# Performance work log

Hardware: AMD Instinct MI355X
Metric: run time of the kernel (lower is better)

Reference implementation:

```python
import jax, jax.numpy as jnp
import numpy as np

N, E, F_IN, H, C, G, NCLS, L = 50000, 600000, 128, 4, 64, 64, 3, 3
HC = H * C  # 256


def gatv2_layer(x, src, dst, Wl, bl, Wr, br, att, bias):
    # PyG GATv2Conv (concat=True, negative_slope=0.2, share_weights=False),
    # eval mode so attention dropout is identity.
    n = x.shape[0]
    xl = (x @ Wl + bl).reshape(n, H, C)  # source transform
    xr = (x @ Wr + br).reshape(n, H, C)  # target transform
    e = jax.nn.leaky_relu(xl[src] + xr[dst], negative_slope=0.2)  # [E',H,C]
    score = jnp.einsum('ehc,hc->eh', e, att)                      # [E',H]
    # softmax over incoming edges of each destination node
    mx = jax.ops.segment_max(score, dst, num_segments=n)
    ex = jnp.exp(score - mx[dst])
    denom = jax.ops.segment_sum(ex, dst, num_segments=n)
    alpha = ex / denom[dst]                                       # [E',H]
    out = jax.ops.segment_sum(alpha[..., None] * xl[src], dst, num_segments=n)
    return out.reshape(n, HC) + bias


def setup_inputs() -> dict:
    key = jax.random.key(0)
    ks = jax.random.split(key, 32)
    d = {}
    d['x'] = jax.random.normal(ks[0], (N, F_IN), dtype=jnp.float32)
    d['edge_index'] = jax.random.randint(ks[1], (2, E), 0, N, dtype=jnp.int64)
    d['batch'] = jnp.sort(jax.random.randint(ks[2], (N,), 0, G, dtype=jnp.int64))
    k = 3
    for li in range(L):
        fin = F_IN if li == 0 else HC
        s = 1.0 / np.sqrt(fin)
        d[f'Wl{li}'] = jax.random.normal(ks[k], (fin, HC), dtype=jnp.float32) * s; k += 1
        d[f'bl{li}'] = jnp.zeros((HC,), dtype=jnp.float32)
        d[f'Wr{li}'] = jax.random.normal(ks[k], (fin, HC), dtype=jnp.float32) * s; k += 1
        d[f'br{li}'] = jnp.zeros((HC,), dtype=jnp.float32)
        d[f'att{li}'] = jax.random.normal(ks[k], (H, C), dtype=jnp.float32) * (1.0 / np.sqrt(C)); k += 1
        d[f'bias{li}'] = jnp.zeros((HC,), dtype=jnp.float32)
    d['Wout'] = jax.random.normal(ks[k], (HC, NCLS), dtype=jnp.float32) * (1.0 / np.sqrt(HC))
    d['bout'] = jnp.zeros((NCLS,), dtype=jnp.float32)
    return d


def reference(x, edge_index, batch,
              Wl0, bl0, Wr0, br0, att0, bias0,
              Wl1, bl1, Wr1, br1, att1, bias1,
              Wl2, bl2, Wr2, br2, att2, bias2,
              Wout, bout):
    # add self loops (add_self_loops=True)
    loops = jnp.arange(N, dtype=edge_index.dtype)
    src = jnp.concatenate([edge_index[0], loops])
    dst = jnp.concatenate([edge_index[1], loops])

    h = gatv2_layer(x, src, dst, Wl0, bl0, Wr0, br0, att0, bias0)
    for (Wl, bl, Wr, br, att, bias) in [(Wl1, bl1, Wr1, br1, att1, bias1),
                                        (Wl2, bl2, Wr2, br2, att2, bias2)]:
        h = jax.nn.relu(h)
        h = gatv2_layer(h, src, dst, Wl, bl, Wr, br, att, bias)

    # pooling=0: mean + max over graphs
    counts = jax.ops.segment_sum(jnp.ones((N,), dtype=h.dtype), batch, num_segments=G)
    mean_p = jax.ops.segment_sum(h, batch, num_segments=G) / jnp.maximum(counts, 1.0)[:, None]
    max_p = jax.ops.segment_max(h, batch, num_segments=G)
    p = mean_p + max_p
    # dropout is identity in eval mode
    logits = p @ Wout + bout
    return jax.nn.softmax(logits, axis=1)
```

## Files before the change

kernel.cpp:

```cpp
#include <hip/hip_runtime.h>
#include <math.h>

#define N_NODES 50000
#define N_EDGES 600000
#define F_INPUT 128
#define HCDIM 256
#define NGRAPH 64
#define NCLS 3
#define MPAD 50048
#define SCAN_NB ((N_NODES + 255) / 256)
#define LOG2E 1.4426950408889634f
#define NPART 32
#define COLX_PAD 16
#define TOTAL_E (N_EDGES + N_NODES)
#define PLANE64 ((size_t)N_NODES * 64)
#define EDGE_CHUNKS ((N_NODES + 63) / 64)
#define DBINS 64
#define BSEG (SCAN_NB / 4)
#define GEMM_NB ((MPAD / 64) * 4)
#define GEMM_QPX (GEMM_NB / 8)

#define FILL_NB   ((TOTAL_E + COLX_PAD + 255) / 256)
#define SPLITX_NB (MPAD * F_INPUT / 4 / 256)
#define ZERO_NB   (((MPAD - N_NODES) * HCDIM / 4 + 255) / 256)
#define WPREP_NB  (512 * (F_INPUT + HCDIM + HCDIM) / 256)
#define PREP_NB   (SPLITX_NB + ZERO_NB + WPREP_NB)
#define HIST_NB   ((N_EDGES + N_NODES + 255) / 256)
#define BND_NB    ((N_NODES + 255) / 256)

typedef float f32x4 __attribute__((ext_vector_type(4)));
typedef float f32x2 __attribute__((ext_vector_type(2)));
typedef _Float16 f16x8 __attribute__((ext_vector_type(8)));
typedef _Float16 f16x4 __attribute__((ext_vector_type(4)));
typedef _Float16 h2 __attribute__((ext_vector_type(2)));

__device__ __forceinline__ void gl_lds16(const void* g, void* l) {
    __builtin_amdgcn_global_load_lds(
        (const __attribute__((address_space(1))) unsigned int*)g,
        (__attribute__((address_space(3))) unsigned int*)l, 16, 0, 0);
}

__device__ __forceinline__ h2 bch2(unsigned int u) { return __builtin_bit_cast(h2, u); }
__device__ __forceinline__ h2 pk16(float a, float b) {
    return __builtin_bit_cast(h2, __builtin_amdgcn_cvt_pkrtz(a, b));
}

__device__ __forceinline__ float quad_reduce_add(float p) {
    int s1 = __builtin_amdgcn_update_dpp(0, __builtin_bit_cast(int, p), 0xB1, 0xF, 0xF, true);
    p += __builtin_bit_cast(float, s1);
    int s2 = __builtin_amdgcn_update_dpp(0, __builtin_bit_cast(int, p), 0x4E, 0xF, 0xF, true);
    p += __builtin_bit_cast(float, s2);
    return p;
}

__global__ void hist_boundary_kernel(const int* __restrict__ ei, int* __restrict__ deg,
                                     const int* __restrict__ batch,
                                     int* __restrict__ startg, int* __restrict__ endg) {
    int b = blockIdx.x;
    if (b < HIST_NB) {
        int i = b * 256 + threadIdx.x;
        int total = N_EDGES + N_NODES;
        if (i >= total) return;
        int d = (i < N_EDGES) ? ei[N_EDGES + i] : (i - N_EDGES);
        atomicAdd(&deg[d], 1);
    } else {
        int i = (b - HIST_NB) * 256 + threadIdx.x;
        if (i >= N_NODES) return;
        int g = batch[i];
        if (i == 0 || batch[i - 1] != g) startg[g] = i;
        if (i == N_NODES - 1 || batch[i + 1] != g) endg[g] = i + 1;
    }
}

__global__ void block_scan_kernel(const int* __restrict__ deg, int* __restrict__ rowptr,
                                  int* __restrict__ bsums) {
    __shared__ int wt[4];
    int b = blockIdx.x, t = threadIdx.x, lane = t & 63, wid = t >> 6;
    int i = b * 256 + t;
    int v = (i < N_NODES) ? deg[i] : 0;
    int x = v;
    #pragma unroll
    for (int off = 1; off < 64; off <<= 1) {
        int y = __shfl_up(x, off, 64);
        if (lane >= off) x += y;
    }
    if (lane == 63) wt[wid] = x;
    __syncthreads();
    if (t == 0) {
        int s = 0;
        #pragma unroll
        for (int j = 0; j < 4; ++j) { int tv = wt[j]; wt[j] = s; s += tv; }
        bsums[b] = s;
    }
    __syncthreads();
    if (i < N_NODES) rowptr[i] = wt[wid] + x - v;
}

__global__ void add_off_kernel(int* __restrict__ rowptr, int* __restrict__ cursor,
                               const int* __restrict__ bsums,
                               const int* __restrict__ deg, int* __restrict__ dhist,
                               int* __restrict__ bcnt) {
    __shared__ int red[256];
    __shared__ int lh[DBINS];
    int b = blockIdx.x, t = threadIdx.x;
    if (t < DBINS) lh[t] = 0;
    red[t] = (t < b) ? bsums[t] : 0;
    __syncthreads();
    for (int off = 128; off > 0; off >>= 1) {
        if (t < off) red[t] += red[t + off];
        __syncthreads();
    }
    int offv = red[0];
    int i = b * 256 + t;
    if (i < N_NODES) {
        int r = rowptr[i] + offv;
        rowptr[i] = r;
        cursor[i] = r;
        int dg = deg[i];
        atomicAdd(&lh[dg < (DBINS - 1) ? dg : (DBINS - 1)], 1);
    }
    if (i == 0) rowptr[N_NODES] = N_EDGES + N_NODES;
    __syncthreads();
    if (t < DBINS) {
        bcnt[b * DBINS + t] = lh[t];
        if (lh[t] != 0) atomicAdd(&dhist[t], lh[t]);
    }
}

__global__ __launch_bounds__(256) void binscan_kernel(const int* __restrict__ dhist,
                                                      int* __restrict__ bcnt) {
    __shared__ int sb[SCAN_NB * DBINS];
    __shared__ int part[4][DBINS];
    __shared__ int binstart[DBINS];
    int t = threadIdx.x;
    for (int i = t; i < SCAN_NB * DBINS; i += 256) sb[i] = bcnt[i];
    if (t < 64) {
        int x = dhist[t];
        #pragma unroll
        for (int off = 1; off < 64; off <<= 1) {
            int y = __shfl_up(x, off, 64);
            if (t >= off) x += y;
        }
        int total = __shfl(x, 63, 64);
        binstart[t] = total - x;
    }
    __syncthreads();
    int l = t & 63, seg = t >> 6;
    int ps = 0;
    for (int b = seg * BSEG; b < (seg + 1) * BSEG; ++b) ps += sb[b * DBINS + l];
    part[seg][l] = ps;
    __syncthreads();
    int off = binstart[l];
    for (int s = 0; s < seg; ++s) off += part[s][l];
    for (int b = seg * BSEG; b < (seg + 1) * BSEG; ++b) {
        int tv = sb[b * DBINS + l];
        sb[b * DBINS + l] = off;
        off += tv;
    }
    __syncthreads();
    for (int i = t; i < SCAN_NB * DBINS; i += 256) bcnt[i] = sb[i];
}

__global__ void prep_fill_kernel(
    const int* __restrict__ ei, int* __restrict__ cursor, int* __restrict__ colx,
    const int* __restrict__ deg, const int* __restrict__ rowptr,
    const int* __restrict__ bcnt, int2* __restrict__ meta,
    const float* __restrict__ x, _Float16* __restrict__ A,
    _Float16* __restrict__ Bt0, _Float16* __restrict__ Bt1, _Float16* __restrict__ Bt2,
    const float* __restrict__ Wl0, const float* __restrict__ Wr0,
    const float* __restrict__ Wl1, const float* __restrict__ Wr1,
    const float* __restrict__ Wl2, const float* __restrict__ Wr2)
{
    int b = blockIdx.x;
    if (b < FILL_NB) {
        __shared__ int lcnt[DBINS];
        int t = threadIdx.x;
        int i = b * 256 + t;
        if (b < SCAN_NB) {
            if (t < DBINS) lcnt[t] = 0;
            __syncthreads();
            if (i < N_NODES) {
                int dg = deg[i];
                int bin = dg < (DBINS - 1) ? dg : (DBINS - 1);
                int myr = atomicAdd(&lcnt[bin], 1);
                int pos = bcnt[b * DBINS + bin] + myr;
                meta[pos] = make_int2(i, rowptr[i] | (dg << 20));
            }
        }
        if (i < TOTAL_E) {
            int s, d;
            if (i < N_EDGES) { s = ei[i]; d = ei[N_EDGES + i]; }
            else             { s = i - N_EDGES; d = s; }
            int pos = atomicAdd(&cursor[d], 1);
            colx[pos] = s * 64;
        } else if (i < TOTAL_E + COLX_PAD) {
            colx[i] = 0;
        }
        return;
    }
    b -= FILL_NB;
    if (b < SPLITX_NB) {
        int base = (b * 256 + threadIdx.x) * 4;
        int row = base >> 7;
        float4 v = make_float4(0.f, 0.f, 0.f, 0.f);
        if (row < N_NODES) v = *(const float4*)&x[base];
        f16x4 o;
        o.x = (_Float16)v.x; o.y = (_Float16)v.y; o.z = (_Float16)v.z; o.w = (_Float16)v.w;
        *(f16x4*)&A[base] = o;
    } else if (b < SPLITX_NB + ZERO_NB) {
        int i = ((b - SPLITX_NB) * 256 + threadIdx.x) * 4;
        if (i < (MPAD - N_NODES) * HCDIM) {
            f16x4 z = {(_Float16)0.f, (_Float16)0.f, (_Float16)0.f, (_Float16)0.f};
            *(f16x4*)&A[(size_t)N_NODES * HCDIM + i] = z;
        }
    } else {
        int t = (b - SPLITX_NB - ZERO_NB) * 256 + threadIdx.x;
        const float* Wl; const float* Wr; _Float16* Bt; int K;
        if (t < 512 * F_INPUT)            { Wl = Wl0; Wr = Wr0; Bt = Bt0; K = F_INPUT; }
        else if (t < 512 * (F_INPUT + HCDIM)) { t -= 512 * F_INPUT; Wl = Wl1; Wr = Wr1; Bt = Bt1; K = HCDIM; }
        else                              { t -= 512 * (F_INPUT + HCDIM); Wl = Wl2; Wr = Wr2; Bt = Bt2; K = HCDIM; }
        int n = t & 511, k = t >> 9;
        float w = (n < 256) ? Wl[k * 256 + n] : Wr[k * 256 + (n - 256)];
        Bt[n * K + k] = (_Float16)w;
    }
}

__global__ __launch_bounds__(256) void gemm_mfma(
    const _Float16* __restrict__ A, const _Float16* __restrict__ B,
    int K,
    const float* __restrict__ bl, const float* __restrict__ br,
    unsigned char* __restrict__ xl8, _Float16* __restrict__ xrh)
{
    __shared__ _Float16 sA[64 * 64], sB[128 * 64];
    int tid = threadIdx.x;
    int lane = tid & 63, wave = tid >> 6;
    int wm = wave >> 1, wn = wave & 1;
    int bid = blockIdx.x;
    int lin = (bid & 7) * GEMM_QPX + (bid >> 3);
    int bx = lin >> 2, by = lin & 3;
    int row0 = bx * 64;
    int n0 = by * 128;
    int quad = lane >> 4, l16 = lane & 15;

    f32x4 acc[2][4];
    #pragma unroll
    for (int i = 0; i < 2; ++i)
        #pragma unroll
        for (int j = 0; j < 4; ++j)
            acc[i][j] = (f32x4){0.f, 0.f, 0.f, 0.f};

    for (int k0 = 0; k0 < K; k0 += 64) {
        __syncthreads();
        #pragma unroll
        for (int pass = 0; pass < 2; ++pass) {
            int c = tid + pass * 256;
            int r = c >> 3;
            int pl = c & 7;
            int pg = pl ^ (r & 7);
            size_t ga = (size_t)(row0 + r) * K + k0 + pg * 8;
            gl_lds16(A + ga, sA + c * 8);
        }
        #pragma unroll
        for (int pass = 0; pass < 4; ++pass) {
            int c = tid + pass * 256;
            int r = c >> 3;
            int pl = c & 7;
            int pg = pl ^ (r & 7);
            size_t gb = (size_t)(n0 + r) * K + k0 + pg * 8;
            gl_lds16(B + gb, sB + c * 8);
        }
        __syncthreads();

        #pragma unroll
        for (int kk = 0; kk < 2; ++kk) {
            f16x8 fa[2], fb[4];
            #pragma unroll
            for (int i = 0; i < 2; ++i) {
                int rr = wm * 32 + i * 16 + l16;
                int ca = (kk * 4 + quad) ^ (rr & 7);
                fa[i] = *(const f16x8*)&sA[rr * 64 + ca * 8];
            }
            #pragma unroll
            for (int j = 0; j < 4; ++j) {
                int nn = wn * 64 + j * 16 + l16;
                int cb = (kk * 4 + quad) ^ (nn & 7);
                fb[j] = *(const f16x8*)&sB[nn * 64 + cb * 8];
            }
            #pragma unroll
            for (int i = 0; i < 2; ++i)
                #pragma unroll
                for (int j = 0; j < 4; ++j)
                    acc[i][j] = __builtin_amdgcn_mfma_f32_16x16x32_f16(fa[i], fb[j], acc[i][j], 0, 0, 0);
        }
    }

    if (by < 2) {
        int cb0 = by * 128;
        #pragma unroll
        for (int j = 0; j < 4; ++j) {
            int col = cb0 + wn * 64 + j * 16 + l16;
            float bj = bl[col];
            int hh = col >> 6, c64 = col & 63;
            unsigned char* xlp = xl8 + (size_t)hh * PLANE64;
            #pragma unroll
            for (int i = 0; i < 2; ++i) {
                int rbase = row0 + wm * 32 + i * 16 + quad * 4;
                #pragma unroll
                for (int r = 0; r < 4; ++r) {
                    int row = rbase + r;
                    if (row < N_NODES) {
                        float v = acc[i][j][r] + bj;
                        int pk = __builtin_amdgcn_cvt_pk_fp8_f32(v, v, 0, false);
                        xlp[(size_t)row * 64 + c64] = (unsigned char)pk;
                    }
                }
            }
        }
    } else {
        int cb0 = (by - 2) * 128;
        #pragma unroll
        for (int j = 0; j < 4; ++j) {
            int col = cb0 + wn * 64 + j * 16 + l16;
            float bj = br[col];
            int hh = col >> 6, c64 = col & 63;
            _Float16* xrp = xrh + (size_t)hh * PLANE64;
            #pragma unroll
            for (int i = 0; i < 2; ++i) {
                int rbase = row0 + wm * 32 + i * 16 + quad * 4;
                #pragma unroll
                for (int r = 0; r < 4; ++r) {
                    int row = rbase + r;
                    if (row < N_NODES)
                        xrp[(size_t)row * 64 + c64] = (_Float16)(acc[i][j][r] + bj);
                }
            }
        }
    }
}

__global__ __launch_bounds__(256) void gat_edge(
    const unsigned char* __restrict__ xl8, const _Float16* __restrict__ xrh,
    const float* __restrict__ att, const float* __restrict__ bias,
    const int2* __restrict__ meta, const int* __restrict__ colx,
    _Float16* __restrict__ outh, _Float16* __restrict__ onext, int mode)
{
    int head = blockIdx.x & 3;
    int chunk = blockIdx.x >> 2;
    int wave = threadIdx.x >> 6;
    int lane = threadIdx.x & 63;
    int g  = lane >> 2;
    int ll = lane & 3;
    int slot = chunk * 64 + wave * 16 + g;
    bool valid = slot < N_NODES;
    int saddr = valid ? slot : 0;
    int2 m = meta[saddr];
    int node = m.x;
    int e0 = m.y & 0xFFFFF;
    int cnt = valid ? (int)((unsigned)m.y >> 20) : 0;
    int ch0 = head * 64 + ll * 16;

    int niter = cnt;
    niter = max(niter, __shfl_xor(niter, 4, 64));
    niter = max(niter, __shfl_xor(niter, 8, 64));
    niter = max(niter, __shfl_xor(niter, 16, 64));
    niter = max(niter, __shfl_xor(niter, 32, 64));

    const char* xrrow = (const char*)(xrh + (size_t)head * PLANE64)
                        + ((size_t)node * 64 + ll * 16) * 2;
    uint4 xu0 = *(const uint4*)xrrow;
    uint4 xu1 = *(const uint4*)(xrrow + 16);
    h2 xr[8] = { bch2(xu0.x), bch2(xu0.y), bch2(xu0.z), bch2(xu0.w),
                 bch2(xu1.x), bch2(xu1.y), bch2(xu1.z), bch2(xu1.w) };
    h2 at[8];
    #pragma unroll
    for (int i = 0; i < 8; ++i) {
        float2 av = *(const float2*)&att[ch0 + i * 2];
        at[i] = (h2){(_Float16)(av.x * LOG2E), (_Float16)(av.y * LOG2E)};
    }

    float denom = 0.f;
    f32x2 accp[8];
    #pragma unroll
    for (int i = 0; i < 8; ++i) accp[i] = (f32x2){0.f, 0.f};

    const unsigned char* xb = xl8 + (size_t)head * PLANE64 + ll * 16;
    const h2 slope = {(_Float16)0.2f, (_Float16)0.2f};

    auto process = [&](uint4 dd, int i) {
        unsigned int dw[4] = {dd.x, dd.y, dd.z, dd.w};
        f32x2 lo[4], hi[4];
        h2 hx[8];
        #pragma unroll
        for (int j = 0; j < 4; ++j) {
            lo[j] = __builtin_amdgcn_cvt_pk_f32_fp8(dw[j], false);
            hi[j] = __builtin_amdgcn_cvt_pk_f32_fp8(dw[j], true);
            hx[2 * j]     = pk16(lo[j].x, lo[j].y);
            hx[2 * j + 1] = pk16(hi[j].x, hi[j].y);
        }
        float pa = 0.f, pb = 0.f;
        #pragma unroll
        for (int j = 0; j < 4; ++j) {
            h2 va = hx[j] + xr[j];
            h2 vb = hx[j + 4] + xr[j + 4];
            va = __builtin_elementwise_max(va, va * slope);
            vb = __builtin_elementwise_max(vb, vb * slope);
            pa = __builtin_amdgcn_fdot2(va, at[j], pa, false);
            pb = __builtin_amdgcn_fdot2(vb, at[j + 4], pb, false);
        }
        float p = quad_reduce_add(pa + pb);
        float w = (i < cnt) ? exp2f(p) : 0.f;
        denom += w;
        f32x2 wp = {w, w};
        #pragma unroll
        for (int j = 0; j < 4; ++j) {
            accp[2 * j]     += wp * lo[j];
            accp[2 * j + 1] += wp * hi[j];
        }
    };

    int cx0 = colx[e0];
// ... 90 lines not shown
    float s = 0.f, m = -INFINITY;
    #pragma unroll 8
    for (int part = 0; part < NPART; ++part) {
        size_t o = (size_t)(g * NPART + part) * HCDIM + c;
        s += sumP[o];
        m = fmaxf(m, maxP[o]);
    }
    int cnt = endg[g] - startg[g];
    float inv = 1.f / fmaxf((float)cnt, 1.f);
    float pv = s * inv + m;

    for (int j = 0; j < NCLS; ++j) {
        red[c] = pv * Wout[c * NCLS + j];
        __syncthreads();
        for (int off = 128; off > 0; off >>= 1) {
            if (c < off) red[c] += red[c + off];
            __syncthreads();
        }
        if (c == 0) lg[j] = red[0] + bout[j];
        __syncthreads();
    }
    if (c == 0) {
        float mx = fmaxf(lg[0], fmaxf(lg[1], lg[2]));
        float e0 = __expf(lg[0] - mx), e1 = __expf(lg[1] - mx), e2 = __expf(lg[2] - mx);
        float invs = 1.f / (e0 + e1 + e2);
        out[g * NCLS + 0] = e0 * invs;
        out[g * NCLS + 1] = e1 * invs;
        out[g * NCLS + 2] = e2 * invs;
    }
}

extern "C" void kernel_launch(void* const* d_in, const int* in_sizes, int n_in,
                              void* d_out, int out_size, void* d_ws, size_t ws_size,
                              hipStream_t stream) {
    const float* x     = (const float*)d_in[0];
    const int*   ei    = (const int*)d_in[1];
    const int*   batch = (const int*)d_in[2];
    const float *Wl[3], *bl[3], *Wr[3], *br[3], *att[3], *bias[3];
    for (int li = 0; li < 3; ++li) {
        int b = 3 + li * 6;
        Wl[li]   = (const float*)d_in[b + 0];
        bl[li]   = (const float*)d_in[b + 1];
        Wr[li]   = (const float*)d_in[b + 2];
        br[li]   = (const float*)d_in[b + 3];
        att[li]  = (const float*)d_in[b + 4];
        bias[li] = (const float*)d_in[b + 5];
    }
    const float* Wout = (const float*)d_in[21];
    const float* bout = (const float*)d_in[22];
    float* out = (float*)d_out;

    size_t off = 0;
    char* wsb = (char*)d_ws;
    auto alloc = [&](size_t bytes) -> char* {
        char* ptr = wsb + off;
        off += (bytes + 255) & ~(size_t)255;
        return ptr;
    };
    int* zblk    = (int*)alloc((N_NODES + 2 * NGRAPH + DBINS) * sizeof(int));
    int* deg     = zblk;
    int* startg  = zblk + N_NODES;
    int* endg    = zblk + N_NODES + NGRAPH;
    int* dhist   = zblk + N_NODES + 2 * NGRAPH;
    int* rowptr  = (int*)alloc((N_NODES + 1) * sizeof(int));
    int* cursor  = (int*)alloc(N_NODES * sizeof(int));
    int* bsums   = (int*)alloc(256 * sizeof(int));
    int* bcnt    = (int*)alloc(SCAN_NB * DBINS * sizeof(int));
    int2* meta   = (int2*)alloc(N_NODES * sizeof(int2));
    int* colx    = (int*)alloc((size_t)(N_EDGES + N_NODES + COLX_PAD) * sizeof(int));
    _Float16* Abuf = (_Float16*)alloc((size_t)MPAD * HCDIM * sizeof(_Float16));
    _Float16* Bt[3];
    for (int li = 0; li < 3; ++li) {
        int K = (li == 0) ? F_INPUT : HCDIM;
        Bt[li] = (_Float16*)alloc((size_t)512 * K * sizeof(_Float16));
    }
    unsigned char* xl8 = (unsigned char*)alloc((size_t)N_NODES * HCDIM);
    _Float16* xrh  = (_Float16*)alloc((size_t)N_NODES * HCDIM * sizeof(_Float16));
    _Float16* hbuf = (_Float16*)alloc((size_t)N_NODES * HCDIM * sizeof(_Float16));
    float* sumP    = (float*)alloc((size_t)NGRAPH * NPART * HCDIM * sizeof(float));
    float* maxP    = (float*)alloc((size_t)NGRAPH * NPART * HCDIM * sizeof(float));

    hipMemsetAsync(zblk, 0, (N_NODES + 2 * NGRAPH + DBINS) * sizeof(int), stream);

    hist_boundary_kernel<<<HIST_NB + BND_NB, 256, 0, stream>>>(ei, deg, batch, startg, endg);
    block_scan_kernel<<<SCAN_NB, 256, 0, stream>>>(deg, rowptr, bsums);
    add_off_kernel<<<SCAN_NB, 256, 0, stream>>>(rowptr, cursor, bsums, deg, dhist, bcnt);
    binscan_kernel<<<1, 256, 0, stream>>>(dhist, bcnt);
    prep_fill_kernel<<<FILL_NB + PREP_NB, 256, 0, stream>>>(
        ei, cursor, colx, deg, rowptr, bcnt, meta,
        x, Abuf, Bt[0], Bt[1], Bt[2],
        Wl[0], Wr[0], Wl[1], Wr[1], Wl[2], Wr[2]);

    for (int li = 0; li < 3; ++li) {
        int K = (li == 0) ? F_INPUT : HCDIM;
        gemm_mfma<<<GEMM_NB, 256, 0, stream>>>(
            Abuf, Bt[li], K, bl[li], br[li], xl8, xrh);
        if (li < 2) {
            gat_edge<<<EDGE_CHUNKS * 4, 256, 0, stream>>>(
                xl8, xrh, att[li], bias[li], meta, colx, nullptr, Abuf, 1);
        } else {
            gat_edge<<<EDGE_CHUNKS * 4, 256, 0, stream>>>(
                xl8, xrh, att[li], bias[li], meta, colx, hbuf, nullptr, 0);
        }
    }

    pool_partial<<<NGRAPH * NPART, 256, 0, stream>>>(hbuf, startg, endg, sumP, maxP);
    pool_final_logits<<<NGRAPH, 256, 0, stream>>>(sumP, maxP, startg, endg, Wout, bout, out);
}
```

Measured before the change: 423.2 us.

## Move input prep into histogram kernel and fuse CSR fill with first GEMM

The x-to-fp16 conversion and weight transposition move into the histogram/boundary kernel, so the first-layer GEMM no longer has to wait for the scan chain before its inputs are ready. The CSR fill blocks and the layer-0 GEMM blocks are merged into one launch, which removes one kernel launch and lets the independent edge fill and GEMM work run concurrently. In exchange, the GEMM code is duplicated with K fixed at 128, and the fill blocks now reserve the GEMM's larger shared memory, which may lower their occupancy.

```diff
diff --git a/kernel.cpp b/kernel.cpp
--- a/kernel.cpp
+++ b/kernel.cpp
@@ -20,13 +20,14 @@
 #define GEMM_NB ((MPAD / 64) * 4)
 #define GEMM_QPX (GEMM_NB / 8)
 
-#define FILL_NB   ((TOTAL_E + COLX_PAD + 255) / 256)
+#define HIST_NB   ((N_EDGES + N_NODES + 255) / 256)
+#define BND_NB    ((N_NODES + 255) / 256)
 #define SPLITX_NB (MPAD * F_INPUT / 4 / 256)
 #define ZERO_NB   (((MPAD - N_NODES) * HCDIM / 4 + 255) / 256)
 #define WPREP_NB  (512 * (F_INPUT + HCDIM + HCDIM) / 256)
-#define PREP_NB   (SPLITX_NB + ZERO_NB + WPREP_NB)
-#define HIST_NB   ((N_EDGES + N_NODES + 255) / 256)
-#define BND_NB    ((N_NODES + 255) / 256)
+#define HP_NB     (HIST_NB + BND_NB + SPLITX_NB + ZERO_NB + WPREP_NB)
+#define FILL_NB   ((TOTAL_E + COLX_PAD + 255) / 256)
+#define FG_NB     (FILL_NB + GEMM_NB)
 
 typedef float f32x4 __attribute__((ext_vector_type(4)));
 typedef float f32x2 __attribute__((ext_vector_type(2)));
@@ -53,22 +54,56 @@
     return p;
 }
 
-__global__ void hist_boundary_kernel(const int* __restrict__ ei, int* __restrict__ deg,
-                                     const int* __restrict__ batch,
-                                     int* __restrict__ startg, int* __restrict__ endg) {
+__global__ void hist_prep_kernel(
+    const int* __restrict__ ei, int* __restrict__ deg,
+    const int* __restrict__ batch, int* __restrict__ startg, int* __restrict__ endg,
+    const float* __restrict__ x, _Float16* __restrict__ A,
+    _Float16* __restrict__ Bt0, _Float16* __restrict__ Bt1, _Float16* __restrict__ Bt2,
+    const float* __restrict__ Wl0, const float* __restrict__ Wr0,
+    const float* __restrict__ Wl1, const float* __restrict__ Wr1,
+    const float* __restrict__ Wl2, const float* __restrict__ Wr2)
+{
     int b = blockIdx.x;
     if (b < HIST_NB) {
         int i = b * 256 + threadIdx.x;
-        int total = N_EDGES + N_NODES;
-        if (i >= total) return;
+        if (i >= TOTAL_E) return;
         int d = (i < N_EDGES) ? ei[N_EDGES + i] : (i - N_EDGES);
         atomicAdd(&deg[d], 1);
-    } else {
-        int i = (b - HIST_NB) * 256 + threadIdx.x;
+        return;
+    }
+    b -= HIST_NB;
+    if (b < BND_NB) {
+        int i = b * 256 + threadIdx.x;
         if (i >= N_NODES) return;
         int g = batch[i];
         if (i == 0 || batch[i - 1] != g) startg[g] = i;
         if (i == N_NODES - 1 || batch[i + 1] != g) endg[g] = i + 1;
+        return;
+    }
+    b -= BND_NB;
+    if (b < SPLITX_NB) {
+        int base = (b * 256 + threadIdx.x) * 4;
+        int row = base >> 7;
+        float4 v = make_float4(0.f, 0.f, 0.f, 0.f);
+        if (row < N_NODES) v = *(const float4*)&x[base];
+        f16x4 o;
+        o.x = (_Float16)v.x; o.y = (_Float16)v.y; o.z = (_Float16)v.z; o.w = (_Float16)v.w;
+        *(f16x4*)&A[base] = o;
+    } else if (b < SPLITX_NB + ZERO_NB) {
+        int i = ((b - SPLITX_NB) * 256 + threadIdx.x) * 4;
+        if (i < (MPAD - N_NODES) * HCDIM) {
+            f16x4 z = {(_Float16)0.f, (_Float16)0.f, (_Float16)0.f, (_Float16)0.f};
+            *(f16x4*)&A[(size_t)N_NODES * HCDIM + i] = z;
+        }
+    } else {
+        int t = (b - SPLITX_NB - ZERO_NB) * 256 + threadIdx.x;
+        const float* Wl; const float* Wr; _Float16* Bt; int K;
+        if (t < 512 * F_INPUT)            { Wl = Wl0; Wr = Wr0; Bt = Bt0; K = F_INPUT; }
+        else if (t < 512 * (F_INPUT + HCDIM)) { t -= 512 * F_INPUT; Wl = Wl1; Wr = Wr1; Bt = Bt1; K = HCDIM; }
+        else                              { t -= 512 * (F_INPUT + HCDIM); Wl = Wl2; Wr = Wr2; Bt = Bt2; K = HCDIM; }
+        int n = t & 511, k = t >> 9;
+        float w = (n < 256) ? Wl[k * 256 + n] : Wr[k * 256 + (n - 256)];
+        Bt[n * K + k] = (_Float16)w;
     }
 }
 
@@ -161,29 +196,28 @@
     for (int i = t; i < SCAN_NB * DBINS; i += 256) bcnt[i] = sb[i];
 }
 
-__global__ void prep_fill_kernel(
+__global__ __launch_bounds__(256) void fill_gemm_kernel(
     const int* __restrict__ ei, int* __restrict__ cursor, int* __restrict__ colx,
     const int* __restrict__ deg, const int* __restrict__ rowptr,
     const int* __restrict__ bcnt, int2* __restrict__ meta,
-    const float* __restrict__ x, _Float16* __restrict__ A,
-    _Float16* __restrict__ Bt0, _Float16* __restrict__ Bt1, _Float16* __restrict__ Bt2,
-    const float* __restrict__ Wl0, const float* __restrict__ Wr0,
-    const float* __restrict__ Wl1, const float* __restrict__ Wr1,
-    const float* __restrict__ Wl2, const float* __restrict__ Wr2)
+    const _Float16* __restrict__ A, const _Float16* __restrict__ B,
+    const float* __restrict__ bl, const float* __restrict__ br,
+    unsigned char* __restrict__ xl8, _Float16* __restrict__ xrh)
 {
-    int b = blockIdx.x;
-    if (b < FILL_NB) {
-        __shared__ int lcnt[DBINS];
+    __shared__ _Float16 sA[64 * 64], sB[128 * 64];
+    int bid = blockIdx.x;
+    if (bid < FILL_NB) {
+        int* lcnt = (int*)sA;
         int t = threadIdx.x;
-        int i = b * 256 + t;
-        if (b < SCAN_NB) {
+        int i = bid * 256 + t;
+        if (bid < SCAN_NB) {
             if (t < DBINS) lcnt[t] = 0;
             __syncthreads();
             if (i < N_NODES) {
                 int dg = deg[i];
                 int bin = dg < (DBINS - 1) ? dg : (DBINS - 1);
                 int myr = atomicAdd(&lcnt[bin], 1);
-                int pos = bcnt[b * DBINS + bin] + myr;
+                int pos = bcnt[bid * DBINS + bin] + myr;
                 meta[pos] = make_int2(i, rowptr[i] | (dg << 20));
             }
         }
@@ -198,30 +232,110 @@
         }
         return;
     }
-    b -= FILL_NB;
-    if (b < SPLITX_NB) {
-        int base = (b * 256 + threadIdx.x) * 4;
-        int row = base >> 7;
-        float4 v = make_float4(0.f, 0.f, 0.f, 0.f);
-        if (row < N_NODES) v = *(const float4*)&x[base];
-        f16x4 o;
-        o.x = (_Float16)v.x; o.y = (_Float16)v.y; o.z = (_Float16)v.z; o.w = (_Float16)v.w;
-        *(f16x4*)&A[base] = o;
-    } else if (b < SPLITX_NB + ZERO_NB) {
-        int i = ((b - SPLITX_NB) * 256 + threadIdx.x) * 4;
-        if (i < (MPAD - N_NODES) * HCDIM) {
-            f16x4 z = {(_Float16)0.f, (_Float16)0.f, (_Float16)0.f, (_Float16)0.f};
-            *(f16x4*)&A[(size_t)N_NODES * HCDIM + i] = z;
+    const int K = F_INPUT;
+    int gbid = bid - FILL_NB;
+    int lin = (gbid & 7) * GEMM_QPX + (gbid >> 3);
+    int bx = lin >> 2, by = lin & 3;
+    int tid = threadIdx.x;
+    int lane = tid & 63, wave = tid >> 6;
+    int wm = wave >> 1, wn = wave & 1;
+    int row0 = bx * 64;
+    int n0 = by * 128;
+    int quad = lane >> 4, l16 = lane & 15;
+
+    f32x4 acc[2][4];
+    #pragma unroll
+    for (int i = 0; i < 2; ++i)
+        #pragma unroll
+        for (int j = 0; j < 4; ++j)
+            acc[i][j] = (f32x4){0.f, 0.f, 0.f, 0.f};
+
+    for (int k0 = 0; k0 < K; k0 += 64) {
+        __syncthreads();
+        #pragma unroll
+        for (int pass = 0; pass < 2; ++pass) {
+            int c = tid + pass * 256;
+            int r = c >> 3;
+            int pl = c & 7;
+            int pg = pl ^ (r & 7);
+            size_t ga = (size_t)(row0 + r) * K + k0 + pg * 8;
+            gl_lds16(A + ga, sA + c * 8);
+        }
+        #pragma unroll
+        for (int pass = 0; pass < 4; ++pass) {
+            int c = tid + pass * 256;
+            int r = c >> 3;
+            int pl = c & 7;
+            int pg = pl ^ (r & 7);
+            size_t gb = (size_t)(n0 + r) * K + k0 + pg * 8;
+            gl_lds16(B + gb, sB + c * 8);
+        }
+        __syncthreads();
+
+        #pragma unroll
+        for (int kk = 0; kk < 2; ++kk) {
+            f16x8 fa[2], fb[4];
+            #pragma unroll
+            for (int i = 0; i < 2; ++i) {
+                int rr = wm * 32 + i * 16 + l16;
+                int ca = (kk * 4 + quad) ^ (rr & 7);
+                fa[i] = *(const f16x8*)&sA[rr * 64 + ca * 8];
+            }
+            #pragma unroll
+            for (int j = 0; j < 4; ++j) {
+                int nn = wn * 64 + j * 16 + l16;
+                int cb = (kk * 4 + quad) ^ (nn & 7);
+                fb[j] = *(const f16x8*)&sB[nn * 64 + cb * 8];
+            }
+            #pragma unroll
+            for (int i = 0; i < 2; ++i)
+                #pragma unroll
+                for (int j = 0; j < 4; ++j)
+                    acc[i][j] = __builtin_amdgcn_mfma_f32_16x16x32_f16(fa[i], fb[j], acc[i][j], 0, 0, 0);
+        }
+    }
+
+    if (by < 2) {
+        int cb0 = by * 128;
+        #pragma unroll
+        for (int j = 0; j < 4; ++j) {
+            int col = cb0 + wn * 64 + j * 16 + l16;
+            float bj = bl[col];
+            int hh = col >> 6, c64 = col & 63;
+            unsigned char* xlp = xl8 + (size_t)hh * PLANE64;
+            #pragma unroll
+            for (int i = 0; i < 2; ++i) {
+                int rbase = row0 + wm * 32 + i * 16 + quad * 4;
+                #pragma unroll
+                for (int r = 0; r < 4; ++r) {
+                    int row = rbase + r;
+                    if (row < N_NODES) {
+                        float v = acc[i][j][r] + bj;
+                        int pk = __builtin_amdgcn_cvt_pk_fp8_f32(v, v, 0, false);
+                        xlp[(size_t)row * 64 + c64] = (unsigned char)pk;
+                    }
+                }
+            }
         }
     } else {
-        int t = (b - SPLITX_NB - ZERO_NB) * 256 + threadIdx.x;
-        const float* Wl; const float* Wr; _Float16* Bt; int K;
-        if (t < 512 * F_INPUT)            { Wl = Wl0; Wr = Wr0; Bt = Bt0; K = F_INPUT; }
-        else if (t < 512 * (F_INPUT + HCDIM)) { t -= 512 * F_INPUT; Wl = Wl1; Wr = Wr1; Bt = Bt1; K = HCDIM; }
-        else                              { t -= 512 * (F_INPUT + HCDIM); Wl = Wl2; Wr = Wr2; Bt = Bt2; K = HCDIM; }
-        int n = t & 511, k = t >> 9;
-        float w = (n < 256) ? Wl[k * 256 + n] : Wr[k * 256 + (n - 256)];
-        Bt[n * K + k] = (_Float16)w;
+        int cb0 = (by - 2) * 128;
+        #pragma unroll
+        for (int j = 0; j < 4; ++j) {
+            int col = cb0 + wn * 64 + j * 16 + l16;
+            float bj = br[col];
+            int hh = col >> 6, c64 = col & 63;
+            _Float16* xrp = xrh + (size_t)hh * PLANE64;
+            #pragma unroll
+            for (int i = 0; i < 2; ++i) {
+                int rbase = row0 + wm * 32 + i * 16 + quad * 4;
+                #pragma unroll
+                for (int r = 0; r < 4; ++r) {
+                    int row = rbase + r;
+                    if (row < N_NODES)
+                        xrp[(size_t)row * 64 + c64] = (_Float16)(acc[i][j][r] + bj);
+                }
+            }
+        }
     }
 }
 
@@ -592,19 +706,23 @@
 
     hipMemsetAsync(zblk, 0, (N_NODES + 2 * NGRAPH + DBINS) * sizeof(int), stream);
 
-    hist_boundary_kernel<<<HIST_NB + BND_NB, 256, 0, stream>>>(ei, deg, batch, startg, endg);
+    hist_prep_kernel<<<HP_NB, 256, 0, stream>>>(
+        ei, deg, batch, startg, endg,
+        x, Abuf, Bt[0], Bt[1], Bt[2],
+        Wl[0], Wr[0], Wl[1], Wr[1], Wl[2], Wr[2]);
     block_scan_kernel<<<SCAN_NB, 256, 0, stream>>>(deg, rowptr, bsums);
     add_off_kernel<<<SCAN_NB, 256, 0, stream>>>(rowptr, cursor, bsums, deg, dhist, bcnt);
     binscan_kernel<<<1, 256, 0, stream>>>(dhist, bcnt);
-    prep_fill_kernel<<<FILL_NB + PREP_NB, 256, 0, stream>>>(
+
+    fill_gemm_kernel<<<FG_NB, 256, 0, stream>>>(
         ei, cursor, colx, deg, rowptr, bcnt, meta,
-        x, Abuf, Bt[0], Bt[1], Bt[2],
-        Wl[0], Wr[0], Wl[1], Wr[1], Wl[2], Wr[2]);
-
-    for (int li = 0; li < 3; ++li) {
-        int K = (li == 0) ? F_INPUT : HCDIM;
+        Abuf, Bt[0], bl[0], br[0], xl8, xrh);
+    gat_edge<<<EDGE_CHUNKS * 4, 256, 0, stream>>>(
+        xl8, xrh, att[0], bias[0], meta, colx, nullptr, Abuf, 1);
+
+    for (int li = 1; li < 3; ++li) {
         gemm_mfma<<<GEMM_NB, 256, 0, stream>>>(
-            Abuf, Bt[li], K, bl[li], br[li], xl8, xrh);
+            Abuf, Bt[li], HCDIM, bl[li], br[li], xl8, xrh);
         if (li < 2) {
             gat_edge<<<EDGE_CHUNKS * 4, 256, 0, stream>>>(
                 xl8, xrh, att[li], bias[li], meta, colx, nullptr, Abuf, 1);
```

New measurement: 411.6 us. 1.03x faster.

## Fuse CSR fill with layer-0 GEMM and enlarge GEMM tile to 128 rows

Applied to the files above, without the earlier changes.

The x/weight prep work moves into the histogram kernel, and the CSR fill now shares one launch with the first-layer GEMM, so the independent fill and GEMM blocks overlap and one launch is dropped. The GEMM tile grows from 64x128 to 128x128 per block, doubling accumulators per wave for more reuse of each B tile. Block-to-tile mapping now uses a general XCD swizzle that handles non-multiple-of-8 grid sizes. Costs are higher register and LDS use per block, which lowers occupancy, and fewer GEMM blocks to spread across CUs.

```diff
diff --git a/kernel.cpp b/kernel.cpp
--- a/kernel.cpp
+++ b/kernel.cpp
@@ -17,16 +17,16 @@
 #define EDGE_CHUNKS ((N_NODES + 63) / 64)
 #define DBINS 64
 #define BSEG (SCAN_NB / 4)
-#define GEMM_NB ((MPAD / 64) * 4)
-#define GEMM_QPX (GEMM_NB / 8)
-
-#define FILL_NB   ((TOTAL_E + COLX_PAD + 255) / 256)
+#define GEMM_NB ((MPAD / 128) * 4)
+
+#define HIST_NB   ((N_EDGES + N_NODES + 255) / 256)
+#define BND_NB    ((N_NODES + 255) / 256)
 #define SPLITX_NB (MPAD * F_INPUT / 4 / 256)
 #define ZERO_NB   (((MPAD - N_NODES) * HCDIM / 4 + 255) / 256)
 #define WPREP_NB  (512 * (F_INPUT + HCDIM + HCDIM) / 256)
-#define PREP_NB   (SPLITX_NB + ZERO_NB + WPREP_NB)
-#define HIST_NB   ((N_EDGES + N_NODES + 255) / 256)
-#define BND_NB    ((N_NODES + 255) / 256)
+#define HP_NB     (HIST_NB + BND_NB + SPLITX_NB + ZERO_NB + WPREP_NB)
+#define FILL_NB   ((TOTAL_E + COLX_PAD + 255) / 256)
+#define FG_NB     (FILL_NB + GEMM_NB)
 
 typedef float f32x4 __attribute__((ext_vector_type(4)));
 typedef float f32x2 __attribute__((ext_vector_type(2)));
@@ -43,6 +43,12 @@
 __device__ __forceinline__ h2 bch2(unsigned int u) { return __builtin_bit_cast(h2, u); }
 __device__ __forceinline__ h2 pk16(float a, float b) {
     return __builtin_bit_cast(h2, __builtin_amdgcn_cvt_pkrtz(a, b));
+}
+
+__device__ __forceinline__ int xcd_swizzle(int bid, int nwg) {
+    int c = bid & 7, idx = bid >> 3;
+    int q = nwg >> 3, r = nwg & 7;
+    return (c < r) ? c * (q + 1) + idx : r * (q + 1) + (c - r) * q + idx;
 }
 
 __device__ __forceinline__ float quad_reduce_add(float p) {
@@ -53,118 +59,118 @@
     return p;
 }
 
-__global__ void hist_boundary_kernel(const int* __restrict__ ei, int* __restrict__ deg,
-                                     const int* __restrict__ batch,
-                                     int* __restrict__ startg, int* __restrict__ endg) {
-    int b = blockIdx.x;
-    if (b < HIST_NB) {
-        int i = b * 256 + threadIdx.x;
-        int total = N_EDGES + N_NODES;
-        if (i >= total) return;
-        int d = (i < N_EDGES) ? ei[N_EDGES + i] : (i - N_EDGES);
-        atomicAdd(&deg[d], 1);
+__device__ __forceinline__ void gemm_body_128(
+    const _Float16* __restrict__ A, const _Float16* __restrict__ B, int K,
+    const float* __restrict__ bl, const float* __restrict__ br,
+    unsigned char* __restrict__ xl8, _Float16* __restrict__ xrh,
+    _Float16* sA, _Float16* sB, int bx, int by)
+{
+    int tid = threadIdx.x;
+    int lane = tid & 63, wave = tid >> 6;
+    int wm = wave >> 1, wn = wave & 1;
+    int row0 = bx * 128;
+    int n0 = by * 128;
+    int quad = lane >> 4, l16 = lane & 15;
+
+    f32x4 acc[4][4];
+    #pragma unroll
+    for (int i = 0; i < 4; ++i)
+        #pragma unroll
+        for (int j = 0; j < 4; ++j)
+            acc[i][j] = (f32x4){0.f, 0.f, 0.f, 0.f};
+
+    for (int k0 = 0; k0 < K; k0 += 64) {
+        __syncthreads();
+        #pragma unroll
+        for (int pass = 0; pass < 4; ++pass) {
+            int c = tid + pass * 256;
+            int r = c >> 3;
+            int pl = c & 7;
+            int pg = pl ^ (r & 7);
+            size_t ga = (size_t)(row0 + r) * K + k0 + pg * 8;
+            gl_lds16(A + ga, sA + c * 8);
+        }
+        #pragma unroll
+        for (int pass = 0; pass < 4; ++pass) {
+            int c = tid + pass * 256;
+            int r = c >> 3;
+            int pl = c & 7;
+            int pg = pl ^ (r & 7);
+            size_t gb = (size_t)(n0 + r) * K + k0 + pg * 8;
+            gl_lds16(B + gb, sB + c * 8);
+        }
+        __syncthreads();
+
+        #pragma unroll
+        for (int kk = 0; kk < 2; ++kk) {
+            f16x8 fa[4], fb[4];
+            #pragma unroll
+            for (int i = 0; i < 4; ++i) {
+                int rr = wm * 64 + i * 16 + l16;
+                int ca = (kk * 4 + quad) ^ (rr & 7);
+                fa[i] = *(const f16x8*)&sA[rr * 64 + ca * 8];
+            }
+            #pragma unroll
+            for (int j = 0; j < 4; ++j) {
+                int nn = wn * 64 + j * 16 + l16;
+                int cb = (kk * 4 + quad) ^ (nn & 7);
+                fb[j] = *(const f16x8*)&sB[nn * 64 + cb * 8];
+            }
+            #pragma unroll
+            for (int i = 0; i < 4; ++i)
+                #pragma unroll
+                for (int j = 0; j < 4; ++j)
+                    acc[i][j] = __builtin_amdgcn_mfma_f32_16x16x32_f16(fa[i], fb[j], acc[i][j], 0, 0, 0);
+        }
+    }
+
+    if (by < 2) {
+        int cb0 = by * 128;
+        #pragma unroll
+        for (int j = 0; j < 4; ++j) {
+            int col = cb0 + wn * 64 + j * 16 + l16;
+            float bj = bl[col];
+            int hh = col >> 6, c64 = col & 63;
+            unsigned char* xlp = xl8 + (size_t)hh * PLANE64;
+            #pragma unroll
+            for (int i = 0; i < 4; ++i) {
+                int rbase = row0 + wm * 64 + i * 16 + quad * 4;
+                #pragma unroll
+                for (int r = 0; r < 4; ++r) {
+                    int row = rbase + r;
+                    if (row < N_NODES) {
+                        float v = acc[i][j][r] + bj;
+                        int pk = __builtin_amdgcn_cvt_pk_fp8_f32(v, v, 0, false);
+                        xlp[(size_t)row * 64 + c64] = (unsigned char)pk;
+                    }
+                }
+            }
+        }
     } else {
-        int i = (b - HIST_NB) * 256 + threadIdx.x;
-        if (i >= N_NODES) return;
-        int g = batch[i];
-        if (i == 0 || batch[i - 1] != g) startg[g] = i;
-        if (i == N_NODES - 1 || batch[i + 1] != g) endg[g] = i + 1;
-    }
-}
-
-__global__ void block_scan_kernel(const int* __restrict__ deg, int* __restrict__ rowptr,
-                                  int* __restrict__ bsums) {
-    __shared__ int wt[4];
-    int b = blockIdx.x, t = threadIdx.x, lane = t & 63, wid = t >> 6;
-    int i = b * 256 + t;
-    int v = (i < N_NODES) ? deg[i] : 0;
-    int x = v;
-    #pragma unroll
-    for (int off = 1; off < 64; off <<= 1) {
-        int y = __shfl_up(x, off, 64);
-        if (lane >= off) x += y;
-    }
-    if (lane == 63) wt[wid] = x;
-    __syncthreads();
-    if (t == 0) {
-        int s = 0;
-        #pragma unroll
-        for (int j = 0; j < 4; ++j) { int tv = wt[j]; wt[j] = s; s += tv; }
-        bsums[b] = s;
-    }
-    __syncthreads();
-    if (i < N_NODES) rowptr[i] = wt[wid] + x - v;
-}
-
-__global__ void add_off_kernel(int* __restrict__ rowptr, int* __restrict__ cursor,
-                               const int* __restrict__ bsums,
-                               const int* __restrict__ deg, int* __restrict__ dhist,
-                               int* __restrict__ bcnt) {
-    __shared__ int red[256];
-    __shared__ int lh[DBINS];
-    int b = blockIdx.x, t = threadIdx.x;
-    if (t < DBINS) lh[t] = 0;
-    red[t] = (t < b) ? bsums[t] : 0;
-    __syncthreads();
-    for (int off = 128; off > 0; off >>= 1) {
-        if (t < off) red[t] += red[t + off];
-        __syncthreads();
-    }
-    int offv = red[0];
-    int i = b * 256 + t;
-    if (i < N_NODES) {
-        int r = rowptr[i] + offv;
-        rowptr[i] = r;
-        cursor[i] = r;
-        int dg = deg[i];
-        atomicAdd(&lh[dg < (DBINS - 1) ? dg : (DBINS - 1)], 1);
-    }
-    if (i == 0) rowptr[N_NODES] = N_EDGES + N_NODES;
-    __syncthreads();
-    if (t < DBINS) {
-        bcnt[b * DBINS + t] = lh[t];
-        if (lh[t] != 0) atomicAdd(&dhist[t], lh[t]);
-    }
-}
-
-__global__ __launch_bounds__(256) void binscan_kernel(const int* __restrict__ dhist,
-                                                      int* __restrict__ bcnt) {
-    __shared__ int sb[SCAN_NB * DBINS];
-    __shared__ int part[4][DBINS];
-    __shared__ int binstart[DBINS];
-    int t = threadIdx.x;
-    for (int i = t; i < SCAN_NB * DBINS; i += 256) sb[i] = bcnt[i];
-    if (t < 64) {
-        int x = dhist[t];
-        #pragma unroll
-        for (int off = 1; off < 64; off <<= 1) {
-            int y = __shfl_up(x, off, 64);
-            if (t >= off) x += y;
-        }
-        int total = __shfl(x, 63, 64);
-        binstart[t] = total - x;
-    }
-    __syncthreads();
-    int l = t & 63, seg = t >> 6;
-    int ps = 0;
-    for (int b = seg * BSEG; b < (seg + 1) * BSEG; ++b) ps += sb[b * DBINS + l];
-    part[seg][l] = ps;
-    __syncthreads();
-    int off = binstart[l];
-    for (int s = 0; s < seg; ++s) off += part[s][l];
-    for (int b = seg * BSEG; b < (seg + 1) * BSEG; ++b) {
-        int tv = sb[b * DBINS + l];
-        sb[b * DBINS + l] = off;
-        off += tv;
-    }
-    __syncthreads();
-    for (int i = t; i < SCAN_NB * DBINS; i += 256) bcnt[i] = sb[i];
-}
-
-__global__ void prep_fill_kernel(
-    const int* __restrict__ ei, int* __restrict__ cursor, int* __restrict__ colx,
-    const int* __restrict__ deg, const int* __restrict__ rowptr,
-    const int* __restrict__ bcnt, int2* __restrict__ meta,
+        int cb0 = (by - 2) * 128;
+        #pragma unroll
+        for (int j = 0; j < 4; ++j) {
+            int col = cb0 + wn * 64 + j * 16 + l16;
+            float bj = br[col];
+            int hh = col >> 6, c64 = col & 63;
+            _Float16* xrp = xrh + (size_t)hh * PLANE64;
+            #pragma unroll
+            for (int i = 0; i < 4; ++i) {
+                int rbase = row0 + wm * 64 + i * 16 + quad * 4;
+                #pragma unroll
+                for (int r = 0; r < 4; ++r) {
+                    int row = rbase + r;
+                    if (row < N_NODES)
+                        xrp[(size_t)row * 64 + c64] = (_Float16)(acc[i][j][r] + bj);
+                }
+            }
+        }
+    }
+}
+
+__global__ void hist_prep_kernel(
+    const int* __restrict__ ei, int* __restrict__ deg,
+    const int* __restrict__ batch, int* __restrict__ startg, int* __restrict__ endg,
     const float* __restrict__ x, _Float16* __restrict__ A,
     _Float16* __restrict__ Bt0, _Float16* __restrict__ Bt1, _Float16* __restrict__ Bt2,
     const float* __restrict__ Wl0, const float* __restrict__ Wr0,
@@ -172,33 +178,23 @@
     const float* __restrict__ Wl2, const float* __restrict__ Wr2)
 {
     int b = blockIdx.x;
-    if (b < FILL_NB) {
-        __shared__ int lcnt[DBINS];
-        int t = threadIdx.x;
-        int i = b * 256 + t;
-        if (b < SCAN_NB) {
-            if (t < DBINS) lcnt[t] = 0;
-            __syncthreads();
-            if (i < N_NODES) {
-                int dg = deg[i];
-                int bin = dg < (DBINS - 1) ? dg : (DBINS - 1);
-                int myr = atomicAdd(&lcnt[bin], 1);
-                int pos = bcnt[b * DBINS + bin] + myr;
-                meta[pos] = make_int2(i, rowptr[i] | (dg << 20));
-            }
-        }
-        if (i < TOTAL_E) {
-            int s, d;
-            if (i < N_EDGES) { s = ei[i]; d = ei[N_EDGES + i]; }
-            else             { s = i - N_EDGES; d = s; }
-            int pos = atomicAdd(&cursor[d], 1);
-            colx[pos] = s * 64;
-        } else if (i < TOTAL_E + COLX_PAD) {
-            colx[i] = 0;
-        }
+    if (b < HIST_NB) {
+        int i = b * 256 + threadIdx.x;
+        if (i >= TOTAL_E) return;
+        int d = (i < N_EDGES) ? ei[N_EDGES + i] : (i - N_EDGES);
+        atomicAdd(&deg[d], 1);
         return;
     }
-    b -= FILL_NB;
+    b -= HIST_NB;
+    if (b < BND_NB) {
+        int i = b * 256 + threadIdx.x;
+        if (i >= N_NODES) return;
+        int g = batch[i];
+        if (i == 0 || batch[i - 1] != g) startg[g] = i;
+        if (i == N_NODES - 1 || batch[i + 1] != g) endg[g] = i + 1;
+        return;
+    }
+    b -= BND_NB;
     if (b < SPLITX_NB) {
         int base = (b * 256 + threadIdx.x) * 4;
         int row = base >> 7;
@@ -225,117 +221,145 @@
     }
 }
 
+__global__ void block_scan_kernel(const int* __restrict__ deg, int* __restrict__ rowptr,
+                                  int* __restrict__ bsums) {
+    __shared__ int wt[4];
+    int b = blockIdx.x, t = threadIdx.x, lane = t & 63, wid = t >> 6;
+    int i = b * 256 + t;
+    int v = (i < N_NODES) ? deg[i] : 0;
+    int x = v;
+    #pragma unroll
+    for (int off = 1; off < 64; off <<= 1) {
+        int y = __shfl_up(x, off, 64);
+        if (lane >= off) x += y;
+    }
+    if (lane == 63) wt[wid] = x;
+    __syncthreads();
+    if (t == 0) {
+        int s = 0;
+        #pragma unroll
+        for (int j = 0; j < 4; ++j) { int tv = wt[j]; wt[j] = s; s += tv; }
+        bsums[b] = s;
+    }
+    __syncthreads();
+    if (i < N_NODES) rowptr[i] = wt[wid] + x - v;
+}
+
+__global__ void add_off_kernel(int* __restrict__ rowptr, int* __restrict__ cursor,
+                               const int* __restrict__ bsums,
+                               const int* __restrict__ deg, int* __restrict__ dhist,
+                               int* __restrict__ bcnt) {
+    __shared__ int red[256];
+    __shared__ int lh[DBINS];
+    int b = blockIdx.x, t = threadIdx.x;
+    if (t < DBINS) lh[t] = 0;
+    red[t] = (t < b) ? bsums[t] : 0;
+    __syncthreads();
+    for (int off = 128; off > 0; off >>= 1) {
+        if (t < off) red[t] += red[t + off];
+        __syncthreads();
+    }
+    int offv = red[0];
+    int i = b * 256 + t;
+    if (i < N_NODES) {
+        int r = rowptr[i] + offv;
+        rowptr[i] = r;
+        cursor[i] = r;
+        int dg = deg[i];
+        atomicAdd(&lh[dg < (DBINS - 1) ? dg : (DBINS - 1)], 1);
+    }
+    if (i == 0) rowptr[N_NODES] = N_EDGES + N_NODES;
+    __syncthreads();
+    if (t < DBINS) {
+        bcnt[b * DBINS + t] = lh[t];
+        if (lh[t] != 0) atomicAdd(&dhist[t], lh[t]);
+    }
+}
+
+__global__ __launch_bounds__(256) void binscan_kernel(const int* __restrict__ dhist,
+                                                      int* __restrict__ bcnt) {
+    __shared__ int sb[SCAN_NB * DBINS];
+    __shared__ int part[4][DBINS];
+    __shared__ int binstart[DBINS];
+    int t = threadIdx.x;
+    for (int i = t; i < SCAN_NB * DBINS; i += 256) sb[i] = bcnt[i];
+    if (t < 64) {
+        int x = dhist[t];
+        #pragma unroll
+        for (int off = 1; off < 64; off <<= 1) {
+            int y = __shfl_up(x, off, 64);
+            if (t >= off) x += y;
+        }
+        int total = __shfl(x, 63, 64);
+        binstart[t] = total - x;
+    }
+    __syncthreads();
+    int l = t & 63, seg = t >> 6;
+    int ps = 0;
+    for (int b = seg * BSEG; b < (seg + 1) * BSEG; ++b) ps += sb[b * DBINS + l];
+    part[seg][l] = ps;
+    __syncthreads();
+    int off = binstart[l];
+    for (int s = 0; s < seg; ++s) off += part[s][l];
+    for (int b = seg * BSEG; b < (seg + 1) * BSEG; ++b) {
+        int tv = sb[b * DBINS + l];
+        sb[b * DBINS + l] = off;
+        off += tv;
+    }
+    __syncthreads();
+    for (int i = t; i < SCAN_NB * DBINS; i += 256) bcnt[i] = sb[i];
+}
+
+__global__ __launch_bounds__(256) void fill_gemm_kernel(
+    const int* __restrict__ ei, int* __restrict__ cursor, int* __restrict__ colx,
+    const int* __restrict__ deg, const int* __restrict__ rowptr,
+    const int* __restrict__ bcnt, int2* __restrict__ meta,
+    const _Float16* __restrict__ A, const _Float16* __restrict__ B,
+    const float* __restrict__ bl, const float* __restrict__ br,
+    unsigned char* __restrict__ xl8, _Float16* __restrict__ xrh)
+{
+    __shared__ _Float16 sA[128 * 64], sB[128 * 64];
+    int bid = blockIdx.x;
+    if (bid < FILL_NB) {
+        int* lcnt = (int*)sA;
+        int t = threadIdx.x;
+        int i = bid * 256 + t;
+        if (bid < SCAN_NB) {
+            if (t < DBINS) lcnt[t] = 0;
+            __syncthreads();
+            if (i < N_NODES) {
+                int dg = deg[i];
+                int bin = dg < (DBINS - 1) ? dg : (DBINS - 1);
+                int myr = atomicAdd(&lcnt[bin], 1);
+                int pos = bcnt[bid * DBINS + bin] + myr;
+                meta[pos] = make_int2(i, rowptr[i] | (dg << 20));
+            }
+        }
+        if (i < TOTAL_E) {
+            int s, d;
+            if (i < N_EDGES) { s = ei[i]; d = ei[N_EDGES + i]; }
+            else             { s = i - N_EDGES; d = s; }
+            int pos = atomicAdd(&cursor[d], 1);
+            colx[pos] = s * 64;
+        } else if (i < TOTAL_E + COLX_PAD) {
+            colx[i] = 0;
+        }
+        return;
+    }
+    int gbid = bid - FILL_NB;
+    int lin = xcd_swizzle(gbid, GEMM_NB);
+    gemm_body_128(A, B, F_INPUT, bl, br, xl8, xrh, sA, sB, lin >> 2, lin & 3);
+}
+
 __global__ __launch_bounds__(256) void gemm_mfma(
     const _Float16* __restrict__ A, const _Float16* __restrict__ B,
     int K,
     const float* __restrict__ bl, const float* __restrict__ br,
     unsigned char* __restrict__ xl8, _Float16* __restrict__ xrh)
 {
-    __shared__ _Float16 sA[64 * 64], sB[128 * 64];
-    int tid = threadIdx.x;
-    int lane = tid & 63, wave = tid >> 6;
-    int wm = wave >> 1, wn = wave & 1;
-    int bid = blockIdx.x;
-    int lin = (bid & 7) * GEMM_QPX + (bid >> 3);
-    int bx = lin >> 2, by = lin & 3;
-    int row0 = bx * 64;
-    int n0 = by * 128;
-    int quad = lane >> 4, l16 = lane & 15;
-
-    f32x4 acc[2][4];
-    #pragma unroll
-    for (int i = 0; i < 2; ++i)
-        #pragma unroll
-        for (int j = 0; j < 4; ++j)
-            acc[i][j] = (f32x4){0.f, 0.f, 0.f, 0.f};
-
-    for (int k0 = 0; k0 < K; k0 += 64) {
-        __syncthreads();
-        #pragma unroll
-        for (int pass = 0; pass < 2; ++pass) {
-            int c = tid + pass * 256;
-            int r = c >> 3;
-            int pl = c & 7;
-            int pg = pl ^ (r & 7);
-            size_t ga = (size_t)(row0 + r) * K + k0 + pg * 8;
-            gl_lds16(A + ga, sA + c * 8);
-        }
-        #pragma unroll
-        for (int pass = 0; pass < 4; ++pass) {
-            int c = tid + pass * 256;
-            int r = c >> 3;
-            int pl = c & 7;
-            int pg = pl ^ (r & 7);
-            size_t gb = (size_t)(n0 + r) * K + k0 + pg * 8;
-            gl_lds16(B + gb, sB + c * 8);
-        }
-        __syncthreads();
-
-        #pragma unroll
-        for (int kk = 0; kk < 2; ++kk) {
-            f16x8 fa[2], fb[4];
-            #pragma unroll
-            for (int i = 0; i < 2; ++i) {
-                int rr = wm * 32 + i * 16 + l16;
-                int ca = (kk * 4 + quad) ^ (rr & 7);
-                fa[i] = *(const f16x8*)&sA[rr * 64 + ca * 8];
-            }
-            #pragma unroll
-            for (int j = 0; j < 4; ++j) {
-                int nn = wn * 64 + j * 16 + l16;
-                int cb = (kk * 4 + quad) ^ (nn & 7);
-                fb[j] = *(const f16x8*)&sB[nn * 64 + cb * 8];
-            }
-            #pragma unroll
-            for (int i = 0; i < 2; ++i)
-                #pragma unroll
-                for (int j = 0; j < 4; ++j)
-                    acc[i][j] = __builtin_amdgcn_mfma_f32_16x16x32_f16(fa[i], fb[j], acc[i][j], 0, 0, 0);
-        }
-    }
-
-    if (by < 2) {
-        int cb0 = by * 128;
-        #pragma unroll
-        for (int j = 0; j < 4; ++j) {
-            int col = cb0 + wn * 64 + j * 16 + l16;
-            float bj = bl[col];
-            int hh = col >> 6, c64 = col & 63;
-            unsigned char* xlp = xl8 + (size_t)hh * PLANE64;
-            #pragma unroll
-            for (int i = 0; i < 2; ++i) {
-                int rbase = row0 + wm * 32 + i * 16 + quad * 4;
-                #pragma unroll
-                for (int r = 0; r < 4; ++r) {
-                    int row = rbase + r;
-                    if (row < N_NODES) {
-                        float v = acc[i][j][r] + bj;
-                        int pk = __builtin_amdgcn_cvt_pk_fp8_f32(v, v, 0, false);
-                        xlp[(size_t)row * 64 + c64] = (unsigned char)pk;
-                    }
-                }
-            }
-        }
-    } else {
-        int cb0 = (by - 2) * 128;
-        #pragma unroll
-        for (int j = 0; j < 4; ++j) {
-            int col = cb0 + wn * 64 + j * 16 + l16;
-            float bj = br[col];
-            int hh = col >> 6, c64 = col & 63;
-            _Float16* xrp = xrh + (size_t)hh * PLANE64;
-            #pragma unroll
-            for (int i = 0; i < 2; ++i) {
-                int rbase = row0 + wm * 32 + i * 16 + quad * 4;
-                #pragma unroll
-                for (int r = 0; r < 4; ++r) {
-                    int row = rbase + r;
-                    if (row < N_NODES)
-                        xrp[(size_t)row * 64 + c64] = (_Float16)(acc[i][j][r] + bj);
-                }
-            }
-        }
-    }
+    __shared__ _Float16 sA[128 * 64], sB[128 * 64];
+    int lin = xcd_swizzle(blockIdx.x, GEMM_NB);
+    gemm_body_128(A, B, K, bl, br, xl8, xrh, sA, sB, lin >> 2, lin & 3);
 }
 
 __global__ __launch_bounds__(256) void gat_edge(
@@ -592,19 +616,23 @@
 
     hipMemsetAsync(zblk, 0, (N_NODES + 2 * NGRAPH + DBINS) * sizeof(int), stream);
 
-    hist_boundary_kernel<<<HIST_NB + BND_NB, 256, 0, stream>>>(ei, deg, batch, startg, endg);
+    hist_prep_kernel<<<HP_NB, 256, 0, stream>>>(
+        ei, deg, batch, startg, endg,
+        x, Abuf, Bt[0], Bt[1], Bt[2],
+        Wl[0], Wr[0], Wl[1], Wr[1], Wl[2], Wr[2]);
     block_scan_kernel<<<SCAN_NB, 256, 0, stream>>>(deg, rowptr, bsums);
     add_off_kernel<<<SCAN_NB, 256, 0, stream>>>(rowptr, cursor, bsums, deg, dhist, bcnt);
     binscan_kernel<<<1, 256, 0, stream>>>(dhist, bcnt);
-    prep_fill_kernel<<<FILL_NB + PREP_NB, 256, 0, stream>>>(
+
+    fill_gemm_kernel<<<FG_NB, 256, 0, stream>>>(
         ei, cursor, colx, deg, rowptr, bcnt, meta,
-        x, Abuf, Bt[0], Bt[1], Bt[2],
-        Wl[0], Wr[0], Wl[1], Wr[1], Wl[2], Wr[2]);
-
-    for (int li = 0; li < 3; ++li) {
-        int K = (li == 0) ? F_INPUT : HCDIM;
+        Abuf, Bt[0], bl[0], br[0], xl8, xrh);
+    gat_edge<<<EDGE_CHUNKS * 4, 256, 0, stream>>>(
+        xl8, xrh, att[0], bias[0], meta, colx, nullptr, Abuf, 1);
+
+    for (int li = 1; li < 3; ++li) {
         gemm_mfma<<<GEMM_NB, 256, 0, stream>>>(
-            Abuf, Bt[li], K, bl[li], br[li], xl8, xrh);
+            Abuf, Bt[li], HCDIM, bl[li], br[li], xl8, xrh);
         if (li < 2) {
             gat_edge<<<EDGE_CHUNKS * 4, 256, 0, stream>>>(
                 xl8, xrh, att[li], bias[li], meta, colx, nullptr, Abuf, 1);
```

Result: slower. 455.4 us (+7.6%).
